# Kernel tuning notes

Measured on AMD Instinct MI355X. Metric: run time of the kernel, lower is better.

## Reference

```python
import jax, jax.numpy as jnp
import numpy as np

IN_F = 4096
OUT_F = 4096
NNZ = 1_600_000
BATCH = 512


def setup_inputs() -> dict:
    key = jax.random.key(0)
    k_x, k_w, k_b, k_r, k_c = jax.random.split(key, 5)
    x = jax.random.normal(k_x, (BATCH, IN_F), dtype=jnp.float32)
    weight1d = jax.random.normal(k_w, (NNZ,), dtype=jnp.float32) * 0.02
    bias = jax.random.normal(k_b, (OUT_F,), dtype=jnp.float32) * 0.02
    row_idx = jax.random.randint(k_r, (NNZ,), 0, OUT_F, dtype=jnp.int64 if jax.config.jax_enable_x64 else jnp.int32)
    col_idx = jax.random.randint(k_c, (NNZ,), 0, IN_F, dtype=jnp.int64 if jax.config.jax_enable_x64 else jnp.int32)
    return {
        "x": x,
        "weight1d": weight1d,
        "bias": bias,
        "row_idx": row_idx,
        "col_idx": col_idx,
        "in_f": IN_F,
        "out_f": OUT_F,
    }


def reference(x, weight1d, bias, row_idx, col_idx, in_f, out_f):
    # matching torch advanced-index assignment semantics up to duplicate ordering).
    W = jnp.zeros((out_f, in_f), dtype=weight1d.dtype).at[row_idx, col_idx].set(weight1d)
    # F.linear(x, W, bias) = x @ W.T + bias
    return x @ W.T + bias
```

## Files before the change

### kernel.cpp

```cpp
#include <hip/hip_runtime.h>
#include <hip/hip_bf16.h>

typedef unsigned short u16;
typedef unsigned long long u64;
typedef __attribute__((ext_vector_type(4))) float f32x4;
typedef __attribute__((ext_vector_type(8))) short bf16x8;

#define IN_F   4096
#define OUT_F  4096
#define BATCH  512

#define BM 128
#define BN 128
#define BK 64
#define KSPLIT 4
#define KC (IN_F / KSPLIT)
#define NSTEPS (KC / BK)

#define NXCD    8
#define NB      512
#define CHUNK   2048
#define LCAP    16
#define SEGCAP  1024
#define RCAP    640
#define SCAP2   256
#define GOVFCAP (1024*1024)
#define NCTR    (NXCD * NB + 2)

__device__ inline u16 f2bf(float f) {
    __hip_bfloat16 h = __float2bfloat16(f);
    u16 u; __builtin_memcpy(&u, &h, 2); return u;
}

__global__ __launch_bounds__(256) void conv_x(const float* __restrict__ x,
                                              u16* __restrict__ xbf,
                                              int* __restrict__ ctrs) {
    const int tid = threadIdx.x;
    if (blockIdx.x == 0) {
        for (int j = tid; j < NCTR; j += 256) ctrs[j] = 0;
    }
    int i = blockIdx.x * 256 + tid;
    float4 v = ((const float4*)x)[i];
    ushort4 o;
    o.x = f2bf(v.x); o.y = f2bf(v.y); o.z = f2bf(v.z); o.w = f2bf(v.w);
    ((ushort4*)xbf)[i] = o;
}

__global__ __launch_bounds__(256) void bucket_scatter(const int* __restrict__ row,
                                                      const int* __restrict__ col,
                                                      const float* __restrict__ w,
                                                      int* __restrict__ gcur,
                                                      u64* __restrict__ bins,
                                                      int* __restrict__ govf_cnt,
                                                      u64* __restrict__ govf, int nnz) {
    __shared__ u64 lbin[NB][LCAP];
    __shared__ int lcur[NB];
    const int xcd = __builtin_amdgcn_s_getreg(20 | (3 << 11)) & (NXCD - 1);
    const int tid = threadIdx.x;
    lcur[tid] = 0;
    lcur[tid + 256] = 0;
    __syncthreads();

    int base = blockIdx.x * CHUNK + tid * 8;
    if (base + 8 <= nnz) {
        int4 r0 = ((const int4*)(row + base))[0];
        int4 r1 = ((const int4*)(row + base))[1];
        int4 c0 = ((const int4*)(col + base))[0];
        int4 c1 = ((const int4*)(col + base))[1];
        float4 w0 = ((const float4*)(w + base))[0];
        float4 w1 = ((const float4*)(w + base))[1];
        int rs[8] = {r0.x, r0.y, r0.z, r0.w, r1.x, r1.y, r1.z, r1.w};
        int cs[8] = {c0.x, c0.y, c0.z, c0.w, c1.x, c1.y, c1.z, c1.w};
        float wsv[8] = {w0.x, w0.y, w0.z, w0.w, w1.x, w1.y, w1.z, w1.w};
#pragma unroll
        for (int j = 0; j < 8; j++) {
            int rr = rs[j], cc = cs[j], i = base + j;
            u64 wb = (u64)f2bf(wsv[j]);
            int bk = rr >> 3;
            int p = atomicAdd(&lcur[bk], 1);
            if (p < LCAP) {
                lbin[bk][p] = ((u64)i << 32) | ((u64)(rr & 7) << 28) | ((u64)cc << 16) | wb;
            } else {
                int o = atomicAdd(govf_cnt, 1);
                if (o < GOVFCAP) govf[o] = ((u64)i << 40) | ((u64)rr << 28) | ((u64)cc << 16) | wb;
            }
        }
    } else {
        int e = nnz < base + 8 ? nnz : base + 8;
        for (int i = base; i < e; i++) {
            int rr = row[i], cc = col[i];
            u64 wb = (u64)f2bf(w[i]);
            int bk = rr >> 3;
            int p = atomicAdd(&lcur[bk], 1);
            if (p < LCAP) {
                lbin[bk][p] = ((u64)i << 32) | ((u64)(rr & 7) << 28) | ((u64)cc << 16) | wb;
            } else {
                int o = atomicAdd(govf_cnt, 1);
                if (o < GOVFCAP) govf[o] = ((u64)i << 40) | ((u64)rr << 28) | ((u64)cc << 16) | wb;
            }
        }
    }
    __syncthreads();

#pragma unroll
    for (int bb = 0; bb < 2; bb++) {
        int bk = tid + bb * 256;
        int cnt = lcur[bk];
        if (cnt > LCAP) cnt = LCAP;
        if (cnt > 0) {
            int gb = (xcd << 9) | bk;
            int b0 = atomicAdd(&gcur[gb], cnt);
            u64* seg = bins + (size_t)gb * SEGCAP;
            for (int k = 0; k < cnt; k++) {
                u64 e = lbin[bk][k];
                int p = b0 + k;
                if (p < SEGCAP) {
                    seg[p] = e;
                } else {
                    int rr = (bk << 3) | ((int)(e >> 28) & 7);
                    int o = atomicAdd(govf_cnt, 1);
                    if (o < GOVFCAP) govf[o] = ((e >> 32) << 40) | ((u64)rr << 28) | (e & 0x0FFFFFFF);
                }
            }
        }
    }
}

__global__ __launch_bounds__(256) void split_build(const int* __restrict__ gcur,
                                                   const u64* __restrict__ bins,
                                                   const int* __restrict__ govf_cnt,
                                                   const u64* __restrict__ govf,
                                                   u16* __restrict__ Wbf) {
    __shared__ u64 lists[8][RCAP];
    __shared__ u64 stash[SCAP2];
    __shared__ u64 aux[IN_F];
    __shared__ int lcur[8];
    __shared__ int scnt;
    const int bucket = blockIdx.x;
    const int tid = threadIdx.x;
    if (tid < 8) lcur[tid] = 0;
    if (tid == 0) scnt = 0;
    __syncthreads();

#pragma unroll
    for (int xcd = 0; xcd < NXCD; xcd++) {
        int gb = (xcd << 9) | bucket;
        int cnt = gcur[gb];
        if (cnt > SEGCAP) cnt = SEGCAP;
        const u64* seg = bins + (size_t)gb * SEGCAP;
        for (int k = tid; k < cnt; k += 256) {
            u64 e = seg[k];
            int rl = (int)(e >> 28) & 7;
            int p = atomicAdd(&lcur[rl], 1);
            if (p < RCAP) lists[rl][p] = e;
            else { int s = atomicAdd(&scnt, 1); if (s < SCAP2) stash[s] = e; }
        }
    }
    int ovfn = *govf_cnt;
    if (ovfn > GOVFCAP) ovfn = GOVFCAP;
    for (int k = tid; k < ovfn; k += 256) {
        u64 e = govf[k];
        int rr = (int)(e >> 28) & 4095;
        if ((rr >> 3) == bucket) {
            u64 e2 = ((e >> 40) << 32) | ((u64)(rr & 7) << 28) | (e & 0x0FFFFFFF);
            int rl = rr & 7;
            int p = atomicAdd(&lcur[rl], 1);
            if (p < RCAP) lists[rl][p] = e2;
            else { int s = atomicAdd(&scnt, 1); if (s < SCAP2) stash[s] = e2; }
        }
    }
    __syncthreads();
    const int sn = scnt > SCAP2 ? SCAP2 : scnt;

    for (int rl = 0; rl < 8; rl++) {
#pragma unroll
        for (int j = 0; j < 8; j++)
            ((ulonglong2*)aux)[tid * 8 + j] = (ulonglong2){0ull, 0ull};
        __syncthreads();

        int cnt = lcur[rl];
        if (cnt > RCAP) cnt = RCAP;
        for (int k = tid; k < cnt; k += 256) {
            u64 e = lists[rl][k];
            atomicMax(&aux[(int)(e >> 16) & 4095], ((e >> 32) << 16) | (e & 0xFFFF));
        }
        for (int k = tid; k < sn; k += 256) {
            u64 e = stash[k];
            if (((int)(e >> 28) & 7) == rl)
                atomicMax(&aux[(int)(e >> 16) & 4095], ((e >> 32) << 16) | (e & 0xFFFF));
        }
        __syncthreads();

        int rowg = (bucket << 3) | rl;
        int base = tid * 16;
        ushort4 o[4];
#pragma unroll
        for (int j = 0; j < 16; j++)
            ((u16*)o)[j] = (u16)(aux[base + j] & 0xFFFF);
        uint4* dst = (uint4*)(Wbf + (size_t)rowg * IN_F + base);
        dst[0] = ((const uint4*)o)[0];
        dst[1] = ((const uint4*)o)[1];
        __syncthreads();
    }
}

__global__ __launch_bounds__(256) void gemm_part(const u16* __restrict__ A,
                                                 const u16* __restrict__ B,
                                                 u16* __restrict__ part) {
    __shared__ u16 As[2][BM * BK];
    __shared__ u16 Bs[2][BN * BK];
    const int L   = blockIdx.x;
    const int xx  = L & 7;
    const int rst = L >> 3;
    const int m   = rst & 3;
    const int g   = ((rst >> 2) << 3) | xx;
    const int n   = g & 31;
    const int kc  = g >> 5;
    const int m0  = m * BM;
    const int n0  = n * BN;
    const int kt0 = kc * KC;

    const int tid  = threadIdx.x;
    const int lane = tid & 63;
    const int wave = tid >> 6;
    const int wm = wave >> 1, wn = wave & 1;
    const int r15 = lane & 15, khi = lane >> 4;

    const u16* srcA[4]; const u16* srcB[4]; int dstO[4];
#pragma unroll
    for (int it = 0; it < 4; it++) {
        int o = tid * 16 + it * 4096;
        int rr = o >> 7, lblk = (o >> 4) & 7;
        srcA[it] = A + (size_t)(m0 + rr) * IN_F + kt0 + ((lblk ^ (rr & 7)) << 3);
        srcB[it] = B + (size_t)(n0 + rr) * IN_F + kt0 + ((lblk ^ (rr & 7)) << 3);
        dstO[it] = o >> 1;
    }

#define STAGE(buf, kk)                                                               \
    do {                                                                             \
        _Pragma("unroll")                                                            \
        for (int it = 0; it < 4; it++)                                               \
            __builtin_amdgcn_global_load_lds(                                        \
                (const __attribute__((address_space(1))) void*)(srcA[it] + (kk)),    \
                (__attribute__((address_space(3))) void*)(&As[buf][dstO[it]]),       \
                16, 0, 0);                                                           \
        _Pragma("unroll")                                                            \
        for (int it = 0; it < 4; it++)                                               \
            __builtin_amdgcn_global_load_lds(                                        \
                (const __attribute__((address_space(1))) void*)(srcB[it] + (kk)),    \
                (__attribute__((address_space(3))) void*)(&Bs[buf][dstO[it]]),       \
                16, 0, 0);                                                           \
    } while (0)

    f32x4 acc[4][4];
#pragma unroll
    for (int mi = 0; mi < 4; mi++)
#pragma unroll
        for (int nj = 0; nj < 4; nj++) acc[mi][nj] = (f32x4){0.f, 0.f, 0.f, 0.f};

    STAGE(0, 0);

    for (int t = 0; t < NSTEPS; ++t) {
        const int cur = t & 1;
        if (t + 1 < NSTEPS) {
            STAGE(cur ^ 1, (t + 1) * BK);
            asm volatile("s_waitcnt vmcnt(8)" ::: "memory");
        } else {
            asm volatile("s_waitcnt vmcnt(0)" ::: "memory");
        }
        __builtin_amdgcn_s_barrier();

        const char* as = (const char*)&As[cur][0];
        const char* bs = (const char*)&Bs[cur][0];
#pragma unroll
        for (int ks = 0; ks < 2; ks++) {
            bf16x8 a[4], b[4];
#pragma unroll
            for (int mi = 0; mi < 4; mi++) {
                int rowi = wm * 64 + mi * 16 + r15;
                a[mi] = *(const bf16x8*)(as + rowi * 128 + (((ks * 4 + khi) ^ (rowi & 7)) << 4));
            }
#pragma unroll
            for (int nj = 0; nj < 4; nj++) {
                int rowi = wn * 64 + nj * 16 + r15;
                b[nj] = *(const bf16x8*)(bs + rowi * 128 + (((ks * 4 + khi) ^ (rowi & 7)) << 4));
            }
#pragma unroll
            for (int mi = 0; mi < 4; mi++)
#pragma unroll
                for (int nj = 0; nj < 4; nj++)
                    acc[mi][nj] = __builtin_amdgcn_mfma_f32_16x16x32_bf16(a[mi], b[nj], acc[mi][nj], 0, 0, 0);
        }
        __builtin_amdgcn_s_barrier();
    }
#undef STAGE

    u16* P = part + (size_t)kc * BATCH * OUT_F;
#pragma unroll
    for (int nj = 0; nj < 4; nj++) {
        int colg = n0 + wn * 64 + nj * 16 + r15;
#pragma unroll
        for (int mi = 0; mi < 4; mi++) {
#pragma unroll
            for (int j = 0; j < 4; j++) {
                int rowg = m0 + wm * 64 + mi * 16 + khi * 4 + j;
                P[(size_t)rowg * OUT_F + colg] = f2bf(acc[mi][nj][j]);
            }
        }
    }
}

__global__ __launch_bounds__(256) void reduce_bias(const u16* __restrict__ part,
                                                   const float* __restrict__ bias,
                                                   float* __restrict__ y) {
    int i = blockIdx.x * 256 + threadIdx.x;
    const size_t S = (size_t)BATCH * OUT_F / 8;
    float s[8];
#pragma unroll
    for (int e = 0; e < 8; e++) s[e] = 0.f;
#pragma unroll
    for (int k = 0; k < KSPLIT; k++) {
        ushort4 v0 = ((const ushort4*)part)[(i + k * S) * 2 + 0];
        ushort4 v1 = ((const ushort4*)part)[(i + k * S) * 2 + 1];
        unsigned vv[8] = {v0.x, v0.y, v0.z, v0.w, v1.x, v1.y, v1.z, v1.w};
#pragma unroll
        for (int e = 0; e < 8; e++) {
            unsigned u = vv[e] << 16;
            float f; __builtin_memcpy(&f, &u, 4);
            s[e] += f;
        }
    }
    int col = (i * 8) & (OUT_F - 1);
    f32x4 b0 = *(const f32x4*)&bias[col];
    f32x4 b1 = *(const f32x4*)&bias[col + 4];
    f32x4 o0 = {s[0] + b0[0], s[1] + b0[1], s[2] + b0[2], s[3] + b0[3]};
    f32x4 o1 = {s[4] + b1[0], s[5] + b1[1], s[6] + b1[2], s[7] + b1[3]};
    ((f32x4*)y)[i * 2 + 0] = o0;
    ((f32x4*)y)[i * 2 + 1] = o1;
}

extern "C" void kernel_launch(void* const* d_in, const int* in_sizes, int n_in,
                              void* d_out, int out_size, void* d_ws, size_t ws_size,
                              hipStream_t stream) {
    const float* x    = (const float*)d_in[0];
    const float* w1d  = (const float*)d_in[1];
    const float* bias = (const float*)d_in[2];
    const int*   row  = (const int*)d_in[3];
    const int*   col  = (const int*)d_in[4];
    const int nnz = in_sizes[1];

    char* ws        = (char*)d_ws;
    u64*  bins      = (u64*)ws;
    u16*  part      = (u16*)ws;
    int*  gcur      = (int*)(ws + ((size_t)32 << 20));
    int*  govf_cnt  = gcur + NXCD * NB;
    u64*  govf      = (u64*)(ws + ((size_t)33 << 20));
    u16*  Wbf       = (u16*)(ws + ((size_t)64 << 20));
    u16*  xbf       = (u16*)(ws + ((size_t)96 << 20));
    float* y        = (float*)d_out;

    conv_x<<<(BATCH * IN_F / 4) / 256, 256, 0, stream>>>(x, xbf, gcur);
    int nblk = (nnz + CHUNK - 1) / CHUNK;
    bucket_scatter<<<nblk, 256, 0, stream>>>(row, col, w1d, gcur, bins, govf_cnt, govf, nnz);
    split_build<<<NB, 256, 0, stream>>>(gcur, bins, govf_cnt, govf, Wbf);
    gemm_part<<<512, 256, 0, stream>>>(xbf, Wbf, part);
    reduce_bias<<<(BATCH * OUT_F / 8) / 256, 256, 0, stream>>>(part, bias, y);
}
```

Before: 91.65 us.

## Fuse split-K reduction and bias into GEMM via per-tile arrival counters

Removes the separate reduce_bias kernel. Each GEMM block increments a per-output-tile atomic counter after writing its bf16 partial, and the last of the KSPLIT blocks to arrive sums all partials for that tile, adds bias and writes the fp32 output. This saves one kernel launch and lets the reduction overlap with other GEMM blocks, at the cost of threadfences, an atomic per block, and serialized reduction work in the last-arriving blocks. The counters are zeroed by the existing conv_x initialization, which is extended via NCTR.

Result: slower. 169.0 us (+84.4%).

```diff
diff --git a/kernel.cpp b/kernel.cpp
--- a/kernel.cpp
+++ b/kernel.cpp
@@ -16,6 +16,7 @@
 #define KSPLIT 4
 #define KC (IN_F / KSPLIT)
 #define NSTEPS (KC / BK)
+#define NTILES ((BATCH / BM) * (OUT_F / BN))
 
 #define NXCD    8
 #define NB      512
@@ -25,7 +26,7 @@
 #define RCAP    640
 #define SCAP2   256
 #define GOVFCAP (1024*1024)
-#define NCTR    (NXCD * NB + 2)
+#define NCTR    (NXCD * NB + 2 + NTILES)
 
 __device__ inline u16 f2bf(float f) {
     __hip_bfloat16 h = __float2bfloat16(f);
@@ -204,11 +205,15 @@
     }
 }
 
-__global__ __launch_bounds__(256) void gemm_part(const u16* __restrict__ A,
-                                                 const u16* __restrict__ B,
-                                                 u16* __restrict__ part) {
+__global__ __launch_bounds__(256) void gemm_fused(const u16* __restrict__ A,
+                                                  const u16* __restrict__ B,
+                                                  const float* __restrict__ bias,
+                                                  u16* __restrict__ part,
+                                                  int* __restrict__ tilectr,
+                                                  float* __restrict__ y) {
     __shared__ u16 As[2][BM * BK];
     __shared__ u16 Bs[2][BN * BK];
+    __shared__ int done_s;
     const int L   = blockIdx.x;
     const int xx  = L & 7;
     const int rst = L >> 3;
@@ -308,35 +313,47 @@
             }
         }
     }
-}
-
-__global__ __launch_bounds__(256) void reduce_bias(const u16* __restrict__ part,
-                                                   const float* __restrict__ bias,
-                                                   float* __restrict__ y) {
-    int i = blockIdx.x * 256 + threadIdx.x;
-    const size_t S = (size_t)BATCH * OUT_F / 8;
-    float s[8];
-#pragma unroll
-    for (int e = 0; e < 8; e++) s[e] = 0.f;
-#pragma unroll
-    for (int k = 0; k < KSPLIT; k++) {
-        ushort4 v0 = ((const ushort4*)part)[(i + k * S) * 2 + 0];
-        ushort4 v1 = ((const ushort4*)part)[(i + k * S) * 2 + 1];
-        unsigned vv[8] = {v0.x, v0.y, v0.z, v0.w, v1.x, v1.y, v1.z, v1.w};
-#pragma unroll
-        for (int e = 0; e < 8; e++) {
-            unsigned u = vv[e] << 16;
-            float f; __builtin_memcpy(&f, &u, 4);
-            s[e] += f;
-        }
-    }
-    int col = (i * 8) & (OUT_F - 1);
-    f32x4 b0 = *(const f32x4*)&bias[col];
-    f32x4 b1 = *(const f32x4*)&bias[col + 4];
-    f32x4 o0 = {s[0] + b0[0], s[1] + b0[1], s[2] + b0[2], s[3] + b0[3]};
-    f32x4 o1 = {s[4] + b1[0], s[5] + b1[1], s[6] + b1[2], s[7] + b1[3]};
-    ((f32x4*)y)[i * 2 + 0] = o0;
-    ((f32x4*)y)[i * 2 + 1] = o1;
+
+    __threadfence();
+    __syncthreads();
+    if (tid == 0) {
+        int old = atomicAdd(&tilectr[m * 32 + n], 1);
+        done_s = (old == KSPLIT - 1) ? 1 : 0;
+    }
+    __syncthreads();
+    if (done_s) {
+        __threadfence();
+#pragma unroll
+        for (int j = 0; j < 8; j++) {
+            int gi = j * 256 + tid;
+            int r  = gi >> 4;
+            int c8 = gi & 15;
+            size_t addr = (size_t)(m0 + r) * OUT_F + n0 + c8 * 8;
+            float s[8];
+#pragma unroll
+            for (int e = 0; e < 8; e++) s[e] = 0.f;
+#pragma unroll
+            for (int k = 0; k < KSPLIT; k++) {
+                const u16* p = part + (size_t)k * BATCH * OUT_F + addr;
+                ushort4 v0 = ((const ushort4*)p)[0];
+                ushort4 v1 = ((const ushort4*)p)[1];
+                unsigned vv[8] = {v0.x, v0.y, v0.z, v0.w, v1.x, v1.y, v1.z, v1.w};
+#pragma unroll
+                for (int e = 0; e < 8; e++) {
+                    unsigned u = vv[e] << 16;
+                    float f; __builtin_memcpy(&f, &u, 4);
+                    s[e] += f;
+                }
+            }
+            int col = n0 + c8 * 8;
+            f32x4 b0 = *(const f32x4*)&bias[col];
+            f32x4 b1 = *(const f32x4*)&bias[col + 4];
+            f32x4 o0 = {s[0] + b0[0], s[1] + b0[1], s[2] + b0[2], s[3] + b0[3]};
+            f32x4 o1 = {s[4] + b1[0], s[5] + b1[1], s[6] + b1[2], s[7] + b1[3]};
+            ((f32x4*)(y + addr))[0] = o0;
+            ((f32x4*)(y + addr))[1] = o1;
+        }
+    }
 }
 
 extern "C" void kernel_launch(void* const* d_in, const int* in_sizes, int n_in,
@@ -354,6 +371,7 @@
     u16*  part      = (u16*)ws;
     int*  gcur      = (int*)(ws + ((size_t)32 << 20));
     int*  govf_cnt  = gcur + NXCD * NB;
+    int*  tilectr   = govf_cnt + 2;
     u64*  govf      = (u64*)(ws + ((size_t)33 << 20));
     u16*  Wbf       = (u16*)(ws + ((size_t)64 << 20));
     u16*  xbf       = (u16*)(ws + ((size_t)96 << 20));
@@ -363,6 +381,5 @@
     int nblk = (nnz + CHUNK - 1) / CHUNK;
     bucket_scatter<<<nblk, 256, 0, stream>>>(row, col, w1d, gcur, bins, govf_cnt, govf, nnz);
     split_build<<<NB, 256, 0, stream>>>(gcur, bins, govf_cnt, govf, Wbf);
-    gemm_part<<<512, 256, 0, stream>>>(xbf, Wbf, part);
-    reduce_bias<<<(BATCH * OUT_F / 8) / 256, 256, 0, stream>>>(part, bias, y);
-}
+    gemm_fused<<<512, 256, 0, stream>>>(xbf, Wbf, bias, part, tilectr, y);
+}
```
